# Optimization experiments

Measured on AMD Instinct MI355X. Metric: run time of the kernel, lower is better.

The kernel has to match this reference:

```python
import jax, jax.numpy as jnp
import numpy as np

N_NODES = 100000
N_HEDGES = 25000
NNZ = 1600000
IN_CH = 128
HEADS_OUT = 128  # heads * out_channels = 8 * 16


def setup_inputs() -> dict:
    key = jax.random.key(0)
    k1, k2, k3, k4, k5, k6 = jax.random.split(key, 6)
    X = jax.random.normal(k1, (N_NODES, IN_CH), dtype=jnp.float32)
    Wlin = jax.random.normal(k2, (IN_CH, HEADS_OUT), dtype=jnp.float32) * (1.0 / np.sqrt(IN_CH))
    degE = jax.random.uniform(k3, (N_HEDGES, 1), dtype=jnp.float32)
    degV = jax.random.uniform(k4, (N_NODES, 1), dtype=jnp.float32)
    W = jnp.ones((N_HEDGES, 1), dtype=jnp.float32)
    g1_src = jax.random.randint(k5, (NNZ,), 0, N_NODES, dtype=jnp.int32)
    g1_dst = jax.random.randint(k6, (NNZ,), 0, N_HEDGES, dtype=jnp.int32)
    return {"X": X, "Wlin": Wlin, "degE": degE, "degV": degV, "W": W,
            "g1_src": g1_src, "g1_dst": g1_dst}


def reference(X, Wlin, degE, degV, W, g1_src, g1_dst):
    # Linear projection (no bias): [N, in_ch] @ [in_ch, heads*out] -> [N, HO]
    Xp = X @ Wlin
    # Stage 1: copy_u_sum over g1 (node -> hyperedge): out[e] = sum_{v in e} Xp[v]
    Xe = jax.ops.segment_sum(Xp[g1_src], g1_dst, num_segments=N_HEDGES)
    # Elementwise hyperedge scaling: degE then W (W is ones buffer in original)
    Xe = Xe * degE * W
    # Stage 2: copy_u_sum over g2 = g1^T (hyperedge -> node)
    Xv = jax.ops.segment_sum(Xe[g1_dst], g1_src, num_segments=N_NODES)
    # Node degree scaling
    Xv = Xv * degV
    return Xv
```

## Files before the change

kernel.cpp:

```cpp
#include <hip/hip_runtime.h>
#include <hip/hip_bf16.h>


#define CAPE 128
#define CAPV 64
#define LDK  136
#define RW   6250

typedef __attribute__((ext_vector_type(8))) short bf16x8;
typedef __attribute__((ext_vector_type(4))) float f32x4;
typedef __attribute__((ext_vector_type(8))) float f32x8;

__device__ __forceinline__ unsigned short f32_to_bf16(float f) {
    unsigned int u = __float_as_uint(f);
    u += 0x7FFFu + ((u >> 16) & 1u);
    return (unsigned short)(u >> 16);
}
__device__ __forceinline__ float bf16_to_f32(unsigned short h) {
    return __uint_as_float(((unsigned int)h) << 16);
}


__device__ __forceinline__ void scan_body(unsigned char* __restrict__ h8, int n,
                                          int b, int nch, int* __restrict__ cnt) {
    int run = 0;
    for (int c0 = 0; c0 < nch; c0 += 16) {
        unsigned char v[16];
#pragma unroll
        for (int j = 0; j < 16; ++j)
            v[j] = h8[(long)(c0 + j) * n + b];
        unsigned char w[16];
#pragma unroll
        for (int j = 0; j < 16; ++j) {
            w[j] = (unsigned char)run;
            run += v[j];
        }
#pragma unroll
        for (int j = 0; j < 16; ++j)
            h8[(long)(c0 + j) * n + b] = w[j];
    }
    cnt[b] = run;
}

__device__ __forceinline__ void hist_body(unsigned int* __restrict__ s32,
                                          const int* __restrict__ key, int nnz,
                                          unsigned int* __restrict__ hist,
                                          int n4, int ch, int c, int w0, int w1,
                                          int tid) {
    const int nw = w1 - w0;
    for (int i = tid; i < nw; i += 256) s32[i] = 0;
    __syncthreads();
    int e0 = c * ch, e1 = e0 + ch; if (e1 > nnz) e1 = nnz;
    for (int e = e0 + tid; e < e1; e += 256) {
        int k = key[e];
        int w = k >> 2;
        if (w >= w0 && w < w1)
            atomicAdd(&s32[w - w0], 1u << ((k & 3) * 8));
    }
    __syncthreads();
    for (int i = tid; i < nw; i += 256)
        hist[(long)c * n4 + w0 + i] = s32[i];
}

__device__ __forceinline__ void scatV_body(unsigned int* __restrict__ c32,
                                           const int* __restrict__ src,
                                           const int* __restrict__ dst, int nnz,
                                           const unsigned char* __restrict__ histV8,
                                           unsigned short* __restrict__ adjV,
                                           int nV4, int chv, int c, int r, int tid) {
    const int w0 = r * RW;
    int w1 = w0 + RW; if (w1 > nV4) w1 = nV4;
    const int nw = w1 - w0;
    const unsigned int* brow = (const unsigned int*)histV8 + (long)c * nV4 + w0;
    for (int i = tid; i < nw; i += 256) c32[i] = brow[i];
    __syncthreads();
    int e0 = c * chv, e1 = e0 + chv; if (e1 > nnz) e1 = nnz;
    for (int e = e0 + tid; e < e1; e += 256) {
        int k = src[e];
        int w = k >> 2;
        if (w < w0 || w >= w1) continue;
        int sh = (k & 3) * 8;
        unsigned int old = atomicAdd(&c32[w - w0], 1u << sh);
        int slot = (old >> sh) & 0xFF;
        if (slot < CAPV) adjV[(long)k * CAPV + slot] = (unsigned short)dst[e];
    }
}

__device__ __forceinline__ void gatherE_body(int id, int tid,
                                             const unsigned short* __restrict__ Xp,
                                             const int* __restrict__ cntE,
                                             const int* __restrict__ adjE,
                                             const float* __restrict__ degE,
                                             const float* __restrict__ Wbuf,
                                             unsigned short* __restrict__ Xe,
                                             int nE) {
    int t = id * 256 + tid;
    int e = t >> 4;
    if (e >= nE) return;
    int c = (t & 15) << 3;
    int len = cntE[e];
    if (len > CAPE) len = CAPE;
    const int* adj = adjE + (long)e * CAPE;
    float acc[8];
#pragma unroll
    for (int q = 0; q < 8; ++q) acc[q] = 0.f;

    int i = 0;
    for (; i + 8 <= len; i += 8) {
        int4 a0 = *(const int4*)(adj + i);
        int4 a1 = *(const int4*)(adj + i + 4);
        int v[8] = {a0.x, a0.y, a0.z, a0.w, a1.x, a1.y, a1.z, a1.w};
        bf16x8 h[8];
#pragma unroll
        for (int j = 0; j < 8; ++j)
            h[j] = *(const bf16x8*)(Xp + (long)v[j] * 128 + c);
#pragma unroll
        for (int j = 0; j < 8; ++j)
#pragma unroll
            for (int q = 0; q < 8; ++q)
                acc[q] += bf16_to_f32((unsigned short)h[j][q]);
    }
    for (; i + 4 <= len; i += 4) {
        int4 a0 = *(const int4*)(adj + i);
        int v[4] = {a0.x, a0.y, a0.z, a0.w};
        bf16x8 h[4];
#pragma unroll
        for (int j = 0; j < 4; ++j)
            h[j] = *(const bf16x8*)(Xp + (long)v[j] * 128 + c);
#pragma unroll
        for (int j = 0; j < 4; ++j)
#pragma unroll
            for (int q = 0; q < 8; ++q)
                acc[q] += bf16_to_f32((unsigned short)h[j][q]);
    }
    for (; i < len; ++i) {
        int v = adj[i];
        bf16x8 h = *(const bf16x8*)(Xp + (long)v * 128 + c);
#pragma unroll
        for (int q = 0; q < 8; ++q)
            acc[q] += bf16_to_f32((unsigned short)h[q]);
    }

    float sc = degE[e] * Wbuf[e];
    bf16x8 o;
#pragma unroll
    for (int q = 0; q < 8; ++q) o[q] = (short)f32_to_bf16(acc[q] * sc);
    *(bf16x8*)(Xe + (long)e * 128 + c) = o;
}

__device__ __forceinline__ void gatherV_body(int id, int tid,
                                             const unsigned short* __restrict__ Xe,
                                             const int* __restrict__ cntV,
                                             const unsigned short* __restrict__ adjV,
                                             const float* __restrict__ degV,
                                             float* __restrict__ out,
                                             int vLo, int vHi) {
    int t = id * 256 + tid;
    int v = vLo + (t >> 4);
    if (v >= vHi) return;
    int c = (t & 15) << 3;
    int len = cntV[v];
    if (len > CAPV) len = CAPV;
    const unsigned short* adj = adjV + (long)v * CAPV;
    float acc[8];
#pragma unroll
    for (int q = 0; q < 8; ++q) acc[q] = 0.f;

    int i = 0;
    for (; i + 8 <= len; i += 8) {
        ushort4 a0 = *(const ushort4*)(adj + i);
        ushort4 a1 = *(const ushort4*)(adj + i + 4);
        int e[8] = {a0.x, a0.y, a0.z, a0.w, a1.x, a1.y, a1.z, a1.w};
        bf16x8 h[8];
#pragma unroll
        for (int j = 0; j < 8; ++j)
            h[j] = *(const bf16x8*)(Xe + (long)e[j] * 128 + c);
#pragma unroll
        for (int j = 0; j < 8; ++j)
#pragma unroll
            for (int q = 0; q < 8; ++q)
                acc[q] += bf16_to_f32((unsigned short)h[j][q]);
    }
    for (; i + 4 <= len; i += 4) {
        ushort4 a0 = *(const ushort4*)(adj + i);
        int e[4] = {a0.x, a0.y, a0.z, a0.w};
        bf16x8 h[4];
#pragma unroll
        for (int j = 0; j < 4; ++j)
            h[j] = *(const bf16x8*)(Xe + (long)e[j] * 128 + c);
#pragma unroll
        for (int j = 0; j < 4; ++j)
#pragma unroll
            for (int q = 0; q < 8; ++q)
                acc[q] += bf16_to_f32((unsigned short)h[j][q]);
    }
    for (; i < len; ++i) {
        int e = adj[i];
        bf16x8 h = *(const bf16x8*)(Xe + (long)e * 128 + c);
#pragma unroll
        for (int q = 0; q < 8; ++q)
            acc[q] += bf16_to_f32((unsigned short)h[q]);
    }

    float sc = degV[v];
    f32x8 o;
#pragma unroll
    for (int q = 0; q < 8; ++q) o[q] = acc[q] * sc;
    *(f32x8*)(out + (long)v * 128 + c) = o;
}


__global__ __launch_bounds__(256) void k_init(const float* __restrict__ Wl,
                                              unsigned short* __restrict__ Wt) {
    int idx = blockIdx.x * 256 + threadIdx.x;
    if (idx < 128 * 128) {
        int n = idx >> 7, k = idx & 127;
        Wt[idx] = f32_to_bf16(Wl[k * 128 + n]);
    }
}

__global__ __launch_bounds__(256) void k_gemm_histE(
    const float* __restrict__ X, const unsigned short* __restrict__ Wt,
    unsigned short* __restrict__ Xp, int nrows, int nGemm,
    const int* __restrict__ keyE, int nnz,
    unsigned int* __restrict__ histE32, int nE4, int che, int nchE)
{
    __shared__ union {
        struct { unsigned short Xs[64 * LDK]; unsigned short Wt[128 * LDK]; } g;
        unsigned int s32[RW];
    } sm;

    int bid = blockIdx.x;
    const int tid = threadIdx.x;

    if (bid < nGemm) {
        const int row0 = bid * 64;
        for (int base = tid * 4; base < 64 * 128; base += 1024) {
            int r = base >> 7, c = base & 127;
            float4 v = make_float4(0.f, 0.f, 0.f, 0.f);
            if (row0 + r < nrows) v = *(const float4*)(X + (long)(row0 + r) * 128 + c);
            ushort4 h;
            h.x = f32_to_bf16(v.x); h.y = f32_to_bf16(v.y);
            h.z = f32_to_bf16(v.z); h.w = f32_to_bf16(v.w);
            *(ushort4*)(sm.g.Xs + r * LDK + c) = h;
        }
        for (int base = tid * 4; base < 128 * 128; base += 1024) {
            int n = base >> 7, k = base & 127;
            ushort4 h = *(const ushort4*)(Wt + base);
            *(ushort4*)(sm.g.Wt + n * LDK + k) = h;
        }
        __syncthreads();

        const int w    = tid >> 6;
        const int lane = tid & 63;
        const int m    = lane & 15;
        const int quad = lane >> 4;

        f32x4 acc[8];
#pragma unroll
        for (int ct = 0; ct < 8; ++ct) acc[ct] = (f32x4){0.f, 0.f, 0.f, 0.f};

#pragma unroll
        for (int kk = 0; kk < 4; ++kk) {
            bf16x8 a = *(const bf16x8*)(sm.g.Xs + (w * 16 + m) * LDK + kk * 32 + quad * 8);
#pragma unroll
            for (int ct = 0; ct < 8; ++ct) {
                bf16x8 b = *(const bf16x8*)(sm.g.Wt + (ct * 16 + m) * LDK + kk * 32 + quad * 8);
                acc[ct] = __builtin_amdgcn_mfma_f32_16x16x32_bf16(a, b, acc[ct], 0, 0, 0);
            }
        }
#pragma unroll
        for (int ct = 0; ct < 8; ++ct) {
#pragma unroll
            for (int r = 0; r < 4; ++r) {
                int row = row0 + w * 16 + quad * 4 + r;
                if (row < nrows)
                    Xp[(long)row * 128 + ct * 16 + m] = f32_to_bf16(acc[ct][r]);
            }
        }
        return;
    }

    int c = bid - nGemm;
    if (c < nchE)
        hist_body(sm.s32, keyE, nnz, histE32, nE4, che, c, 0, nE4, tid);
}

__global__ __launch_bounds__(256) void k_scanE_histV(
    unsigned char* __restrict__ histE8, int* __restrict__ cntE,
    int nE, int nchE, int nScanE,
    const int* __restrict__ keyV, int nnz,
    unsigned int* __restrict__ histV32, int nV4, int chv, int nchV)
{
    __shared__ unsigned int s32[RW];
    int bid = blockIdx.x;
    const int tid = threadIdx.x;
    if (bid < nScanE) {
        int t = bid * 256 + tid;
        if (t < nE) scan_body(histE8, nE, t, nchE, cntE);
        return;
    }
    bid -= nScanE;
    const int c = bid % nchV, r = bid / nchV;
    const int w0 = r * RW;
    int w1 = w0 + RW; if (w1 > nV4) w1 = nV4;
    hist_body(s32, keyV, nnz, histV32, nV4, chv, c, w0, w1, tid);
}

__global__ __launch_bounds__(256) void k_scatE_scanV(
    const int* __restrict__ src, const int* __restrict__ dst, int nnz,
    const unsigned char* __restrict__ histE8, int* __restrict__ adjE,
    int nE4, int che, int nchE,
    unsigned char* __restrict__ histV8, int* __restrict__ cntV, int nV, int nchV)
{
    __shared__ unsigned int c32[RW];
    int bid = blockIdx.x;
    const int tid = threadIdx.x;
    if (bid < nchE) {
        const int c = bid;
        const unsigned int* brow = (const unsigned int*)histE8 + (long)c * nE4;
        for (int i = tid; i < nE4; i += 256) c32[i] = brow[i];
        __syncthreads();
        int e0 = c * che, e1 = e0 + che; if (e1 > nnz) e1 = nnz;
        for (int e = e0 + tid; e < e1; e += 256) {
            int k = dst[e];
            int sh = (k & 3) * 8;
            unsigned int old = atomicAdd(&c32[k >> 2], 1u << sh);
            int slot = (old >> sh) & 0xFF;
            if (slot < CAPE) adjE[(long)k * CAPE + slot] = src[e];
        }
        return;
    }
    int t = (bid - nchE) * 256 + tid;
    if (t < nV) scan_body(histV8, nV, t, nchV, cntV);
}

__global__ __launch_bounds__(256) void k_gathE_scatV(
    const unsigned short* __restrict__ Xp, const int* __restrict__ cntE,
    const int* __restrict__ adjE, const float* __restrict__ degE,
    const float* __restrict__ Wbuf, unsigned short* __restrict__ Xe,
    int nE, int nGathE,
    const int* __restrict__ src, const int* __restrict__ dst, int nnz,
    const unsigned char* __restrict__ histV8, unsigned short* __restrict__ adjV,
    int nV4, int chv, int nchV)
{
    __shared__ unsigned int c32[RW];
    int bid = blockIdx.x;
    const int tid = threadIdx.x;
    if (bid < nGathE) {
        gatherE_body(bid, tid, Xp, cntE, adjE, degE, Wbuf, Xe, nE);
        return;
    }
    bid -= nGathE;
    const int c = bid % nchV, r = bid / nchV;
    scatV_body(c32, src, dst, nnz, histV8, adjV, nV4, chv, c, r, tid);
}

__global__ __launch_bounds__(256) void k_gathV_scatV(
    const unsigned short* __restrict__ Xe, const int* __restrict__ cntV,
    const unsigned short* __restrict__ adjV, const float* __restrict__ degV,
    float* __restrict__ out, int vSplit, int nGathV,
    const int* __restrict__ src, const int* __restrict__ dst, int nnz,
    const unsigned char* __restrict__ histV8, unsigned short* __restrict__ adjVw,
    int nV4, int chv, int nchV, int rBase)
{
    __shared__ unsigned int c32[RW];
    int bid = blockIdx.x;
    const int tid = threadIdx.x;
    if (bid < nGathV) {
        gatherV_body(bid, tid, Xe, cntV, adjV, degV, out, 0, vSplit);
        return;
    }
    bid -= nGathV;
    const int c = bid % nchV, r = rBase + bid / nchV;
    scatV_body(c32, src, dst, nnz, histV8, adjVw, nV4, chv, c, r, tid);
}

__global__ __launch_bounds__(256) void k_gatherV(const unsigned short* __restrict__ Xe,
                                                 const int* __restrict__ cntV,
                                                 const unsigned short* __restrict__ adjV,
                                                 const float* __restrict__ degV,
                                                 float* __restrict__ out,
                                                 int vLo, int vHi) {
    gatherV_body(blockIdx.x, threadIdx.x, Xe, cntV, adjV, degV, out, vLo, vHi);
}

__global__ __launch_bounds__(256) void zero_f4(float4* __restrict__ p, int n4) {
    int i = blockIdx.x * 256 + threadIdx.x;
    if (i < n4) p[i] = make_float4(0.f, 0.f, 0.f, 0.f);
}

__global__ __launch_bounds__(256) void gemm_xw_f32(const float* __restrict__ X,
                                                   const float* __restrict__ Wl,
                                                   float* __restrict__ Xp,
                                                   int nrows) {
    __shared__ float Xs[32 * 128];
    const int tid = threadIdx.x;
    const int row0 = blockIdx.x * 32;
    for (int i = tid * 4; i < 32 * 128; i += 256 * 4) {
        int r = row0 + (i >> 7);
        float4 v = make_float4(0.f, 0.f, 0.f, 0.f);
        if (r < nrows) v = *(const float4*)(X + (long)row0 * 128 + i);
        *(float4*)(Xs + i) = v;
    }
    __syncthreads();
    const int col = tid & 127;
    const int rg  = (tid >> 7) * 16;
    float acc[16];
#pragma unroll
    for (int r = 0; r < 16; ++r) acc[r] = 0.f;
    for (int k = 0; k < 128; k += 4) {
        const float w0 = Wl[(k + 0) * 128 + col];
        const float w1 = Wl[(k + 1) * 128 + col];
        const float w2 = Wl[(k + 2) * 128 + col];
        const float w3 = Wl[(k + 3) * 128 + col];
#pragma unroll
        for (int r = 0; r < 16; ++r) {
            float4 x = *(const float4*)(Xs + (rg + r) * 128 + k);
            acc[r] = fmaf(x.w, w3, fmaf(x.z, w2, fmaf(x.y, w1, fmaf(x.x, w0, acc[r]))));
        }
    }
#pragma unroll
    for (int r = 0; r < 16; ++r) {
        int row = row0 + rg + r;
        if (row < nrows) Xp[(long)row * 128 + col] = acc[r];
    }
}

__global__ __launch_bounds__(256) void scatter_to_hedges(const float* __restrict__ Xp,
                                                         const int* __restrict__ src,
                                                         const int* __restrict__ dst,
                                                         float* __restrict__ Xe,
                                                         int nnz) {
    int t = blockIdx.x * 256 + threadIdx.x;
    int e = t >> 5;
    if (e >= nnz) return;
    int c = (t & 31) << 2;
    int s = src[e], d = dst[e];
    float4 v = *(const float4*)(Xp + (long)s * 128 + c);
    float* o = Xe + (long)d * 128 + c;
    atomicAdd(o + 0, v.x); atomicAdd(o + 1, v.y);
    atomicAdd(o + 2, v.z); atomicAdd(o + 3, v.w);
}

__global__ __launch_bounds__(256) void scatter_to_nodes(const float* __restrict__ Xe,
                                                        const int* __restrict__ src,
                                                        const int* __restrict__ dst,
                                                        const float* __restrict__ degE,
                                                        const float* __restrict__ Wbuf,
                                                        const float* __restrict__ degV,
                                                        float* __restrict__ out,
                                                        int nnz) {
    int t = blockIdx.x * 256 + threadIdx.x;
    int e = t >> 5;
    if (e >= nnz) return;
    int c = (t & 31) << 2;
    int s = src[e], d = dst[e];
    float sc = degE[d] * Wbuf[d] * degV[s];
    float4 v = *(const float4*)(Xe + (long)d * 128 + c);
    float* o = out + (long)s * 128 + c;
    atomicAdd(o + 0, v.x * sc); atomicAdd(o + 1, v.y * sc);
    atomicAdd(o + 2, v.z * sc); atomicAdd(o + 3, v.w * sc);
}

extern "C" void kernel_launch(void* const* d_in, const int* in_sizes, int n_in,
                              void* d_out, int out_size, void* d_ws, size_t ws_size,
                              hipStream_t stream) {
    const float* X    = (const float*)d_in[0];
    const float* Wlin = (const float*)d_in[1];
    const float* degE = (const float*)d_in[2];
    const float* degV = (const float*)d_in[3];
    const float* Wbuf = (const float*)d_in[4];
    const int* g1_src = (const int*)d_in[5];
    const int* g1_dst = (const int*)d_in[6];

    const int nE  = in_sizes[2];
    const int nV  = in_sizes[3];
    const int nnz = in_sizes[5];

    float* out = (float*)d_out;
    char* ws = (char*)d_ws;

    auto layout_size = [&](int cE, int cV) -> size_t {
        size_t o = 0;
        o += (size_t)nE * CAPE * 4;
        o += (size_t)nV * CAPV * 2;
        o += (size_t)nE * 4 + (size_t)nV * 4;
        size_t he = (size_t)cE * nE;
        size_t xe = (size_t)nE * 128 * 2;
        o += (he > xe) ? he : xe;
        o += (size_t)cV * nV;
        o += 128 * 128 * 2;
        o += 4096;
        return o;
    };

    int nchE = 256, nchV = 256;
    if (layout_size(nchE, nchV) > ws_size) { nchE = 256; nchV = 128; }
    if (layout_size(nchE, nchV) > ws_size) { nchE = 128; nchV = 128; }
    if (layout_size(nchE, nchV) > ws_size) { nchE = 64;  nchV = 64;  }

    const int nE4 = nE >> 2, nV4 = nV >> 2;
    const bool eligible = ((nE & 3) == 0) && ((nV & 3) == 0) && (nE4 <= RW) &&
                          layout_size(nchE, nchV) <= ws_size;

    if (eligible) {
        size_t boff = 0;
        auto alloc = [&](size_t bytes) -> char* {
            char* p = ws + boff;
            boff += (bytes + 255) & ~(size_t)255;
            return p;
        };
        int* adjE            = (int*)alloc((size_t)nE * CAPE * 4);
        unsigned short* adjV = (unsigned short*)alloc((size_t)nV * CAPV * 2);
        int* cntE            = (int*)alloc((size_t)nE * 4);
        int* cntV            = (int*)alloc((size_t)nV * 4);
        size_t he = (size_t)nchE * nE;
        size_t xe = (size_t)nE * 128 * 2;
        char* region1         = alloc((he > xe) ? he : xe);
        unsigned char* histE8 = (unsigned char*)region1;
        unsigned short* Xe    = (unsigned short*)region1;
        unsigned char* histV8 = (unsigned char*)alloc((size_t)nchV * nV);
        unsigned short* Wt    = (unsigned short*)alloc((size_t)128 * 128 * 2);

        unsigned short* Xp_bf = (unsigned short*)d_out;

        const int nrV    = (nV4 + RW - 1) / RW;
        const int rSplit = (nrV + 1) / 2;
        int vSplit = rSplit * RW * 4; if (vSplit > nV) vSplit = nV;
        const int che = (nnz + nchE - 1) / nchE;
        const int chv = (nnz + nchV - 1) / nchV;

        k_init<<<64, 256, 0, stream>>>(Wlin, Wt);

        int nGemm = (nV + 63) / 64;
        k_gemm_histE<<<nGemm + nchE, 256, 0, stream>>>(
            X, Wt, Xp_bf, nV, nGemm,
            g1_dst, nnz, (unsigned int*)histE8, nE4, che, nchE);

        int nScanE = (nE + 255) / 256;
        k_scanE_histV<<<nScanE + nchV * nrV, 256, 0, stream>>>(
            histE8, cntE, nE, nchE, nScanE,
            g1_src, nnz, (unsigned int*)histV8, nV4, chv, nchV);

        int nScanV = (nV + 255) / 256;
        k_scatE_scanV<<<nchE + nScanV, 256, 0, stream>>>(
            g1_src, g1_dst, nnz, histE8, adjE, nE4, che, nchE,
            histV8, cntV, nV, nchV);

        int nGathE = (nE * 16 + 255) / 256;
        k_gathE_scatV<<<nGathE + nchV * rSplit, 256, 0, stream>>>(
            Xp_bf, cntE, adjE, degE, Wbuf, Xe, nE, nGathE,
            g1_src, g1_dst, nnz, histV8, adjV, nV4, chv, nchV);

        int nGathV1 = (vSplit * 16 + 255) / 256;
        k_gathV_scatV<<<nGathV1 + nchV * (nrV - rSplit), 256, 0, stream>>>(
            Xe, cntV, adjV, degV, out, vSplit, nGathV1,
            g1_src, g1_dst, nnz, histV8, adjV, nV4, chv, nchV, rSplit);

        if (vSplit < nV) {
            int nGathV2 = ((nV - vSplit) * 16 + 255) / 256;
            k_gatherV<<<nGathV2, 256, 0, stream>>>(Xe, cntV, adjV, degV, out,
                                                   vSplit, nV);
        }
    } else {
        float* XeF = (float*)d_ws;
        float* Xp  = out;
        int n4 = nE * 128 / 4;
        zero_f4<<<(n4 + 255) / 256, 256, 0, stream>>>((float4*)XeF, n4);
        gemm_xw_f32<<<(nV + 31) / 32, 256, 0, stream>>>(X, Wlin, Xp, nV);
        long th = (long)nnz * 32;
        scatter_to_hedges<<<(int)((th + 255) / 256), 256, 0, stream>>>(Xp, g1_src, g1_dst,
                                                                       XeF, nnz);
        int m4 = out_size / 4;
        zero_f4<<<(m4 + 255) / 256, 256, 0, stream>>>((float4*)out, m4);
        scatter_to_nodes<<<(int)((th + 255) / 256), 256, 0, stream>>>(XeF, g1_src, g1_dst,
                                                                      degE, Wbuf, degV,
                                                                      out, nnz);
    }
}
```

Measured before the change: 341.0 us.

## Unroll gathers to 16 neighbors and run all node scatter with hyperedge gather

Adds a 16-wide unrolled loop to both gather kernels so each thread keeps more independent row loads in flight. It also stops splitting the node-adjacency scatter across two launches: all scatter row blocks now run alongside the hyperedge gather, and the node gather runs as a single launch afterward. This removes the fused gatherV/scatV kernel and one launch, but loses the overlap of the second half of the scatter with the node gather, and the wider unroll raises register pressure.

```diff
diff --git a/kernel.cpp b/kernel.cpp
--- a/kernel.cpp
+++ b/kernel.cpp
@@ -106,6 +106,23 @@
     for (int q = 0; q < 8; ++q) acc[q] = 0.f;
 
     int i = 0;
+    for (; i + 16 <= len; i += 16) {
+        int4 a0 = *(const int4*)(adj + i);
+        int4 a1 = *(const int4*)(adj + i + 4);
+        int4 a2 = *(const int4*)(adj + i + 8);
+        int4 a3 = *(const int4*)(adj + i + 12);
+        int v[16] = {a0.x, a0.y, a0.z, a0.w, a1.x, a1.y, a1.z, a1.w,
+                     a2.x, a2.y, a2.z, a2.w, a3.x, a3.y, a3.z, a3.w};
+        bf16x8 h[16];
+#pragma unroll
+        for (int j = 0; j < 16; ++j)
+            h[j] = *(const bf16x8*)(Xp + (long)v[j] * 128 + c);
+#pragma unroll
+        for (int j = 0; j < 16; ++j)
+#pragma unroll
+            for (int q = 0; q < 8; ++q)
+                acc[q] += bf16_to_f32((unsigned short)h[j][q]);
+    }
     for (; i + 8 <= len; i += 8) {
         int4 a0 = *(const int4*)(adj + i);
         int4 a1 = *(const int4*)(adj + i + 4);
@@ -167,6 +184,23 @@
     for (int q = 0; q < 8; ++q) acc[q] = 0.f;
 
     int i = 0;
+    for (; i + 16 <= len; i += 16) {
+        ushort4 a0 = *(const ushort4*)(adj + i);
+        ushort4 a1 = *(const ushort4*)(adj + i + 4);
+        ushort4 a2 = *(const ushort4*)(adj + i + 8);
+        ushort4 a3 = *(const ushort4*)(adj + i + 12);
+        int e[16] = {a0.x, a0.y, a0.z, a0.w, a1.x, a1.y, a1.z, a1.w,
+                     a2.x, a2.y, a2.z, a2.w, a3.x, a3.y, a3.z, a3.w};
+        bf16x8 h[16];
+#pragma unroll
+        for (int j = 0; j < 16; ++j)
+            h[j] = *(const bf16x8*)(Xe + (long)e[j] * 128 + c);
+#pragma unroll
+        for (int j = 0; j < 16; ++j)
+#pragma unroll
+            for (int q = 0; q < 8; ++q)
+                acc[q] += bf16_to_f32((unsigned short)h[j][q]);
+    }
     for (; i + 8 <= len; i += 8) {
         ushort4 a0 = *(const ushort4*)(adj + i);
         ushort4 a1 = *(const ushort4*)(adj + i + 4);
@@ -356,26 +390,6 @@
     scatV_body(c32, src, dst, nnz, histV8, adjV, nV4, chv, c, r, tid);
 }
 
-__global__ __launch_bounds__(256) void k_gathV_scatV(
-    const unsigned short* __restrict__ Xe, const int* __restrict__ cntV,
-    const unsigned short* __restrict__ adjV, const float* __restrict__ degV,
-    float* __restrict__ out, int vSplit, int nGathV,
-    const int* __restrict__ src, const int* __restrict__ dst, int nnz,
-    const unsigned char* __restrict__ histV8, unsigned short* __restrict__ adjVw,
-    int nV4, int chv, int nchV, int rBase)
-{
-    __shared__ unsigned int c32[RW];
-    int bid = blockIdx.x;
-    const int tid = threadIdx.x;
-    if (bid < nGathV) {
-        gatherV_body(bid, tid, Xe, cntV, adjV, degV, out, 0, vSplit);
-        return;
-    }
-    bid -= nGathV;
-    const int c = bid % nchV, r = rBase + bid / nchV;
-    scatV_body(c32, src, dst, nnz, histV8, adjVw, nV4, chv, c, r, tid);
-}
-
 __global__ __launch_bounds__(256) void k_gatherV(const unsigned short* __restrict__ Xe,
                                                  const int* __restrict__ cntV,
                                                  const unsigned short* __restrict__ adjV,
@@ -525,9 +539,7 @@
 
         unsigned short* Xp_bf = (unsigned short*)d_out;
 
-        const int nrV    = (nV4 + RW - 1) / RW;
-        const int rSplit = (nrV + 1) / 2;
-        int vSplit = rSplit * RW * 4; if (vSplit > nV) vSplit = nV;
+        const int nrV = (nV4 + RW - 1) / RW;
         const int che = (nnz + nchE - 1) / nchE;
         const int chv = (nnz + nchV - 1) / nchV;
 
@@ -549,20 +561,12 @@
             histV8, cntV, nV, nchV);
 
         int nGathE = (nE * 16 + 255) / 256;
-        k_gathE_scatV<<<nGathE + nchV * rSplit, 256, 0, stream>>>(
+        k_gathE_scatV<<<nGathE + nchV * nrV, 256, 0, stream>>>(
             Xp_bf, cntE, adjE, degE, Wbuf, Xe, nE, nGathE,
             g1_src, g1_dst, nnz, histV8, adjV, nV4, chv, nchV);
 
-        int nGathV1 = (vSplit * 16 + 255) / 256;
-        k_gathV_scatV<<<nGathV1 + nchV * (nrV - rSplit), 256, 0, stream>>>(
-            Xe, cntV, adjV, degV, out, vSplit, nGathV1,
-            g1_src, g1_dst, nnz, histV8, adjV, nV4, chv, nchV, rSplit);
-
-        if (vSplit < nV) {
-            int nGathV2 = ((nV - vSplit) * 16 + 255) / 256;
-            k_gatherV<<<nGathV2, 256, 0, stream>>>(Xe, cntV, adjV, degV, out,
-                                                   vSplit, nV);
-        }
+        int nGathV = (nV * 16 + 255) / 256;
+        k_gatherV<<<nGathV, 256, 0, stream>>>(Xe, cntV, adjV, degV, out, 0, nV);
     } else {
         float* XeF = (float*)d_ws;
         float* Xp  = out;
```

Result: faster. 326.2 us, median of 2 (-4.3%).
